# Kernel optimization log

Hardware: AMD Instinct MI355X
Metric: run time of the kernel (lower is better)

Reference implementation:

```python
import jax, jax.numpy as jnp
import numpy as np
import math

B, C, H, W = 16, 512, 32, 32
HEADS = 8
HD = C // HEADS            # 64 head_dim
NFREQ = HD // 4            # 16 (head_dim % 4 == 0)
MAX_FREQ = 128.0
T = H * W                  # 1024 tokens


def _make_so2_mat():
    # make_2dcoord: meshgrid('ij') of arange(H), arange(W) -> [H, W, 2]
    xg, yg = np.meshgrid(np.arange(H, dtype=np.float32), np.arange(W, dtype=np.float32), indexing='ij')
    coord = np.stack([xg, yg], -1)                                   # [H, W, 2]
    freqs = np.exp(np.linspace(0.0, math.log(MAX_FREQ), NFREQ)).astype(np.float32)  # [NFREQ]
    th = coord[..., None, :] * freqs[None, None, :, None]            # [H, W, NFREQ, 2]
    c, s = np.cos(th), np.sin(th)
    # rotation matrices [[c, -s], [s, c]] -> [H, W, NFREQ, 2(dim), 2, 2]
    mat = np.stack([np.stack([c, -s], -1), np.stack([s, c], -1)], -2)
    mat = mat.reshape(H * W, NFREQ * 2, 2, 2)                        # flatten(2,3) then flatten(0,1)
    return jnp.asarray(mat[:, : HD // 2])                            # [T, HD//2, 2, 2]


def setup_inputs() -> dict:
    key = jax.random.key(0)
    ks = jax.random.split(key, 5)
    mat = _make_so2_mat()
    return {
        'x': jax.random.normal(ks[0], (B, C, H, W), dtype=jnp.float32),
        'w_qkv': jax.random.normal(ks[1], (3 * C, C), dtype=jnp.float32) * 0.02,
        'b_qkv': jax.random.normal(ks[2], (3 * C,), dtype=jnp.float32) * 0.02,
        'w_o': jax.random.normal(ks[3], (C, C), dtype=jnp.float32) * 0.02,
        'b_o': jax.random.normal(ks[4], (C,), dtype=jnp.float32) * 0.02,
        'mat_q': mat,
        'mat_k': mat,
        'mat_v': mat,
        'mat_o': jnp.swapaxes(mat, -2, -1),
    }


def _rep_mul(rep, t):
    # rep: [T, HD//2, 2, 2]; t: [B, nh, T, HD] -> per-pair 2x2 rotation
    tb = t.reshape(B, HEADS, T, HD // 2, 2)
    return jnp.einsum('tfij,bntfj->bntfi', rep, tb).reshape(B, HEADS, T, HD)


def _split_heads(t):
    # 'b (c nh) h w -> b nh (h w) c' (c outer, nh inner in channel dim)
    return t.reshape(B, HD, HEADS, T).transpose(0, 2, 3, 1)


def reference(x, w_qkv, b_qkv, w_o, b_o, mat_q, mat_k, mat_v, mat_o):
    # 1x1 conv QKV projection == channel GEMM
    qkv = jnp.einsum('bchw,oc->bohw', x, w_qkv) + b_qkv[None, :, None, None]
    q, k, v = jnp.split(qkv, 3, axis=1)
    q, k, v = map(_split_heads, (q, k, v))                 # [B, nh, T, HD]
    q = _rep_mul(mat_q, q)
    k = _rep_mul(mat_k, k)
    v = _rep_mul(mat_v, v)
    scale = 1.0 / math.sqrt(HD)
    attn = jax.nn.softmax(jnp.einsum('bntd,bnsd->bnts', q, k) * scale, axis=-1)
    o = jnp.einsum('bnts,bnsd->bntd', attn, v)             # [B, nh, T, HD]
    o = _rep_mul(mat_o, o)
    # 'b nh (h w) c -> b (c nh) h w'
    o = o.reshape(B, HEADS, H, W, HD).transpose(0, 4, 1, 2, 3).reshape(B, C, H, W)
    return jnp.einsum('bchw,oc->bohw', o, w_o) + b_o[None, :, None, None]
```

## Files before the change

kernel.cpp:

```cpp
#include <hip/hip_runtime.h>


typedef __bf16 bf16x8 __attribute__((ext_vector_type(8)));
typedef __bf16 bf16x4 __attribute__((ext_vector_type(4)));
typedef float  f32x4  __attribute__((ext_vector_type(4)));

__device__ __forceinline__ f32x4 mfma16(bf16x8 a, bf16x8 b, f32x4 c) {
    return __builtin_amdgcn_mfma_f32_16x16x32_bf16(a, b, c, 0, 0, 0);
}

__device__ __forceinline__ void async16(const void* g, void* l) {
    __builtin_amdgcn_global_load_lds(
        (const __attribute__((address_space(1))) void*)g,
        (__attribute__((address_space(3))) void*)l, 16, 0, 0);
}

__global__ void k_convert_w(const float* __restrict__ wq, const float* __restrict__ wo,
                            __bf16* __restrict__ wqb, __bf16* __restrict__ wob) {
    int i = blockIdx.x * 256 + threadIdx.x;
    if (i < 3 * 512 * 512) wqb[i] = (__bf16)wq[i];
    if (i < 512 * 512) {
        int o = i >> 9, k2 = i & 511;
        int nh = k2 >> 6, hd = k2 & 63;
        wob[i] = (__bf16)wo[o * 512 + hd * 8 + nh];
    }
}

__global__ void k_transpose_x(const float* __restrict__ x, __bf16* __restrict__ xt) {
    __shared__ float tile[64][65];
    const int b  = blockIdx.z;
    const int c0 = blockIdx.y * 64;
    const int t0 = blockIdx.x * 64;
    const int tx = threadIdx.x, ty = threadIdx.y;
    const float* xp = x + ((size_t)b * 512 + c0) * 1024 + t0;
#pragma unroll
    for (int j = 0; j < 16; j++)
        tile[ty + j * 4][tx] = xp[(ty + j * 4) * 1024 + tx];
    __syncthreads();
    __bf16* xo = xt + ((size_t)b * 1024 + t0) * 512 + c0;
#pragma unroll
    for (int j = 0; j < 16; j++)
        xo[(ty + j * 4) * 512 + tx] = (__bf16)tile[tx][ty + j * 4];
}

__global__ __launch_bounds__(512) void k_gemm_qkv(
        const __bf16* __restrict__ A, const __bf16* __restrict__ W,
        const float* __restrict__ bias,
        const float* __restrict__ matq, const float* __restrict__ matk,
        const float* __restrict__ matv,
        __bf16* __restrict__ qd, __bf16* __restrict__ kd, __bf16* __restrict__ vtd)
{
    __shared__ __bf16 As[2][128][64];
    __shared__ __bf16 Bs[2][256][64];
    const int tid = threadIdx.x;
    const int m0 = blockIdx.x * 128;
    const int jb = blockIdx.y;
    const int part = jb >> 1;
    const int nh_base = (jb & 1) * 4;
    const int lane = tid & 63, w = tid >> 6;
    const int ln = lane & 15, quad = lane >> 4;
    const int wr = w >> 2, wc = w & 3;

    const int srow = lane >> 3;
    const int scol = (((lane & 7) ^ srow) * 8);

    const __bf16* arow[2];
    const __bf16* brow[4];
#pragma unroll
    for (int jj = 0; jj < 2; jj++) {
        int rr = w * 16 + jj * 8 + srow;
        arow[jj] = &A[(size_t)(m0 + rr) * 512 + scol];
    }
#pragma unroll
    for (int jj = 0; jj < 4; jj++) {
        int rr = w * 32 + jj * 8 + srow;
        int o = part * 512 + (rr & 63) * 8 + nh_base + (rr >> 6);
        brow[jj] = &W[(size_t)o * 512 + scol];
    }

    f32x4 acc[4][4] = {};

#define STAGE_QKV(T, BUF)                                                   \
    do {                                                                    \
        const int _k0 = (T) * 64;                                           \
        _Pragma("unroll")                                                   \
        for (int jj = 0; jj < 2; jj++)                                      \
            async16(arow[jj] + _k0, &As[BUF][w * 16 + jj * 8][0]);          \
        _Pragma("unroll")                                                   \
        for (int jj = 0; jj < 4; jj++)                                      \
            async16(brow[jj] + _k0, &Bs[BUF][w * 32 + jj * 8][0]);          \
    } while (0)

    STAGE_QKV(0, 0);
    STAGE_QKV(1, 1);
    asm volatile("s_waitcnt vmcnt(6)" ::: "memory");
    __builtin_amdgcn_s_barrier();

#pragma unroll
    for (int t = 0; t < 8; ++t) {
        const int cur = t & 1;
        bf16x8 af[2][4], wf[2][4];
#pragma unroll
        for (int h = 0; h < 2; h++) {
#pragma unroll
            for (int mi = 0; mi < 4; mi++)
                af[h][mi] = *(const bf16x8*)&As[cur][wr * 64 + mi * 16 + ln][(((h * 4 + quad) ^ (ln & 7)) * 8)];
#pragma unroll
            for (int ni = 0; ni < 4; ni++)
                wf[h][ni] = *(const bf16x8*)&Bs[cur][wc * 64 + ni * 16 + ln][(((h * 4 + quad) ^ (ln & 7)) * 8)];
        }
        asm volatile("s_waitcnt lgkmcnt(0)" ::: "memory");
        __builtin_amdgcn_sched_barrier(0);
        __builtin_amdgcn_s_barrier();
        if (t < 6) STAGE_QKV(t + 2, cur);
        __builtin_amdgcn_s_setprio(1);
#pragma unroll
        for (int h = 0; h < 2; h++)
#pragma unroll
            for (int mi = 0; mi < 4; mi++)
#pragma unroll
                for (int ni = 0; ni < 4; ni++)
                    acc[mi][ni] = mfma16(af[h][mi], wf[h][ni], acc[mi][ni]);
        __builtin_amdgcn_s_setprio(0);
        if (t < 6) { asm volatile("s_waitcnt vmcnt(6)" ::: "memory"); }
        else       { asm volatile("s_waitcnt vmcnt(0)" ::: "memory"); }
        __builtin_amdgcn_s_barrier();
    }
#undef STAGE_QKV

    const int nh = nh_base + wc;
    const int rowbase = m0 + wr * 64;
    const int b  = rowbase >> 10, t0 = rowbase & 1023;
    const int bh = b * 8 + nh;
    const int ip = ln & 1;
    const float2* matp = (const float2*)(part == 0 ? matq : (part == 1 ? matk : matv));
    __bf16* qkdst = (part == 0) ? qd : kd;
    const float qscale = (part == 0) ? 0.18033688011112042f : 1.0f;

#pragma unroll
    for (int ni = 0; ni < 4; ni++) {
        const int hd = ni * 16 + ln;
        const int f  = hd >> 1;
        const float bias_o = bias[part * 512 + hd * 8 + nh];
#pragma unroll
        for (int mi = 0; mi < 4; mi++) {
            const int tq = t0 + mi * 16 + quad * 4;
            if (part < 2) {
#pragma unroll
                for (int r = 0; r < 4; r++) {
                    int t = tq + r;
                    float val = acc[mi][ni][r] + bias_o;
                    float pr  = __shfl_xor(val, 1);
                    float2 mv = matp[((size_t)t * 32 + f) * 2 + ip];
                    float e  = ip ? pr : val;
                    float oo = ip ? val : pr;
                    float rv = (mv.x * e + mv.y * oo) * qscale;
                    qkdst[((size_t)bh * 1024 + t) * 64 + hd] = (__bf16)rv;
                }
            } else {
                __bf16 pack[4];
#pragma unroll
                for (int r = 0; r < 4; r++) {
                    int t = tq + r;
                    float val = acc[mi][ni][r] + bias_o;
                    float pr  = __shfl_xor(val, 1);
                    float2 mv = matp[((size_t)t * 32 + f) * 2 + ip];
                    float e  = ip ? pr : val;
                    float oo = ip ? val : pr;
                    pack[r] = (__bf16)(mv.x * e + mv.y * oo);
                }
                *(uint2*)&vtd[((size_t)bh * 64 + hd) * 1024 + tq] = *(const uint2*)pack;
            }
        }
    }
}

__global__ __launch_bounds__(512) void k_attn(
        const __bf16* __restrict__ q, const __bf16* __restrict__ kk,
        const __bf16* __restrict__ vt, const float* __restrict__ mato,
        __bf16* __restrict__ od)
{
    __shared__ __bf16 Ks[64][64];
    __shared__ __bf16 Vs[64][64];
    __shared__ __bf16 Ps[8][32][64];
    const int bh = blockIdx.x, qt = blockIdx.y;
    const int tid = threadIdx.x, w = tid >> 6, lane = tid & 63;
    const int ln = lane & 15, quad = lane >> 4;
    const int lx = ln & 7;
    const int srow = lane >> 3;
    const int scol = ((lane & 7) ^ srow) * 8;
    const int qr0 = qt * 256 + w * 32;

    bf16x8 qa[2][2];
#pragma unroll
    for (int mi = 0; mi < 2; mi++)
#pragma unroll
        for (int ki = 0; ki < 2; ki++)
            qa[mi][ki] = *(const bf16x8*)&q[((size_t)bh * 1024 + qr0 + mi * 16 + ln) * 64 + ki * 32 + quad * 8];

    const __bf16* kbase = kk + (size_t)bh * 1024 * 64;
    const __bf16* vbase = vt + (size_t)bh * 64 * 1024;

    f32x4 oacc[2][4] = {};
    f32x4 lacc[2] = {};

    bf16x8 ones;
#pragma unroll
    for (int j = 0; j < 8; j++) ones[j] = (__bf16)1.0f;

    for (int st = 0; st < 16; st++) {
        async16(kbase + (size_t)(st * 64 + w * 8 + srow) * 64 + scol, &Ks[w * 8][0]);
        async16(vbase + (size_t)(w * 8 + srow) * 1024 + st * 64 + scol, &Vs[w * 8][0]);
        __syncthreads();

#pragma unroll
        for (int si = 0; si < 4; si++) {
            bf16x8 kb0 = *(const bf16x8*)&Ks[si * 16 + ln][((quad    ) ^ lx) * 8];
            bf16x8 kb1 = *(const bf16x8*)&Ks[si * 16 + ln][((quad + 4) ^ lx) * 8];
            f32x4 sc[2] = {};
#pragma unroll
            for (int mi = 0; mi < 2; mi++) {
                sc[mi] = mfma16(kb0, qa[mi][0], sc[mi]);
                sc[mi] = mfma16(kb1, qa[mi][1], sc[mi]);
            }
#pragma unroll
            for (int mi = 0; mi < 2; mi++) {
                bf16x4 pk;
#pragma unroll
                for (int r = 0; r < 4; r++)
                    pk[r] = (__bf16)exp2f(sc[mi][r]);
                *(bf16x4*)((char*)&Ps[w][mi * 16 + ln][0]
                           + (((si * 2 + (quad >> 1)) ^ lx) * 16) + (quad & 1) * 8) = pk;
            }
        }

#pragma unroll
        for (int kt = 0; kt < 2; kt++) {
            bf16x8 pa[2];
#pragma unroll
            for (int mi = 0; mi < 2; mi++)
                pa[mi] = *(const bf16x8*)&Ps[w][mi * 16 + ln][((kt * 4 + quad) ^ lx) * 8];
#pragma unroll
            for (int ni = 0; ni < 4; ni++) {
                bf16x8 vb = *(const bf16x8*)&Vs[ni * 16 + ln][((kt * 4 + quad) ^ lx) * 8];
                oacc[0][ni] = mfma16(vb, pa[0], oacc[0][ni]);
                oacc[1][ni] = mfma16(vb, pa[1], oacc[1][ni]);
            }
            lacc[0] = mfma16(ones, pa[0], lacc[0]);
            lacc[1] = mfma16(ones, pa[1], lacc[1]);
        }
        __syncthreads();
    }

    const float4* mo4 = (const float4*)mato;
#pragma unroll
    for (int mi = 0; mi < 2; mi++) {
        const int t = qr0 + mi * 16 + ln;
        const float invl = 1.0f / lacc[mi][0];
#pragma unroll
        for (int ni = 0; ni < 4; ni++) {
            const int hd0 = ni * 16 + quad * 4;
            const int f   = hd0 >> 1;
            float v0 = oacc[mi][ni][0] * invl;
            float v1 = oacc[mi][ni][1] * invl;
            float v2 = oacc[mi][ni][2] * invl;
            float v3 = oacc[mi][ni][3] * invl;
            float4 m1 = mo4[(size_t)t * 32 + f];
            float4 m2 = mo4[(size_t)t * 32 + f + 1];
            __bf16 pk[4];
            pk[0] = (__bf16)(m1.x * v0 + m1.y * v1);
            pk[1] = (__bf16)(m1.z * v0 + m1.w * v1);
            pk[2] = (__bf16)(m2.x * v2 + m2.y * v3);
            pk[3] = (__bf16)(m2.z * v2 + m2.w * v3);
            *(uint2*)&od[((size_t)bh * 1024 + t) * 64 + hd0] = *(const uint2*)pk;
        }
    }
}

__global__ __launch_bounds__(512) void k_gemm_out(
        const __bf16* __restrict__ A, const __bf16* __restrict__ W,
        const float* __restrict__ bias, float* __restrict__ out)
{
    __shared__ __bf16 As[2][128][64];
    __shared__ __bf16 Bs[2][256][64];
    const int tid = threadIdx.x;
    const int m0 = blockIdx.x * 128;
    const int n0 = blockIdx.y * 256;
    const int lane = tid & 63, w = tid >> 6;
    const int ln = lane & 15, quad = lane >> 4;
    const int wr = w >> 2, wc = w & 3;

    const int srow = lane >> 3;
    const int scol = (((lane & 7) ^ srow) * 8);

    const int bb = m0 >> 10, t00 = m0 & 1023;

    const __bf16* arow[2];
    const __bf16* brow[4];
#pragma unroll
    for (int jj = 0; jj < 2; jj++) {
        int rr = w * 16 + jj * 8 + srow;
        arow[jj] = &A[((size_t)bb * 8192 + t00 + rr) * 64 + scol];
    }
#pragma unroll
    for (int jj = 0; jj < 4; jj++) {
        int rr = w * 32 + jj * 8 + srow;
        brow[jj] = &W[(size_t)(n0 + rr) * 512 + scol];
    }

    f32x4 acc[4][4] = {};

#define STAGE_OUT(T, BUF)                                                   \
    do {                                                                    \
        const int _k0 = (T) * 64;                                           \
        _Pragma("unroll")                                                   \
        for (int jj = 0; jj < 2; jj++)                                      \
            async16(arow[jj] + (size_t)_k0 * 1024, &As[BUF][w * 16 + jj * 8][0]); \
        _Pragma("unroll")                                                   \
        for (int jj = 0; jj < 4; jj++)                                      \
            async16(brow[jj] + _k0, &Bs[BUF][w * 32 + jj * 8][0]);          \
    } while (0)

    STAGE_OUT(0, 0);
    STAGE_OUT(1, 1);
    asm volatile("s_waitcnt vmcnt(6)" ::: "memory");
    __builtin_amdgcn_s_barrier();

#pragma unroll
    for (int t = 0; t < 8; ++t) {
        const int cur = t & 1;
        bf16x8 af[2][4], wf[2][4];
#pragma unroll
        for (int h = 0; h < 2; h++) {
#pragma unroll
            for (int mi = 0; mi < 4; mi++)
                af[h][mi] = *(const bf16x8*)&As[cur][wr * 64 + mi * 16 + ln][(((h * 4 + quad) ^ (ln & 7)) * 8)];
#pragma unroll
            for (int ni = 0; ni < 4; ni++)
                wf[h][ni] = *(const bf16x8*)&Bs[cur][wc * 64 + ni * 16 + ln][(((h * 4 + quad) ^ (ln & 7)) * 8)];
        }
        asm volatile("s_waitcnt lgkmcnt(0)" ::: "memory");
        __builtin_amdgcn_sched_barrier(0);
        __builtin_amdgcn_s_barrier();
        if (t < 6) STAGE_OUT(t + 2, cur);
        __builtin_amdgcn_s_setprio(1);
#pragma unroll
        for (int h = 0; h < 2; h++)
#pragma unroll
            for (int mi = 0; mi < 4; mi++)
#pragma unroll
                for (int ni = 0; ni < 4; ni++)
                    acc[mi][ni] = mfma16(af[h][mi], wf[h][ni], acc[mi][ni]);
        __builtin_amdgcn_s_setprio(0);
        if (t < 6) { asm volatile("s_waitcnt vmcnt(6)" ::: "memory"); }
        else       { asm volatile("s_waitcnt vmcnt(0)" ::: "memory"); }
        __builtin_amdgcn_s_barrier();
    }
#undef STAGE_OUT

    const int rowbase = m0 + wr * 64;
    const int bb2 = rowbase >> 10, t0 = rowbase & 1023;
#pragma unroll
    for (int ni = 0; ni < 4; ni++) {
        int o = n0 + wc * 64 + ni * 16 + ln;
        float bias_o = bias[o];
#pragma unroll
        for (int mi = 0; mi < 4; mi++) {
            int t = t0 + mi * 16 + quad * 4;
            f32x4 v = acc[mi][ni];
            v[0] += bias_o; v[1] += bias_o; v[2] += bias_o; v[3] += bias_o;
            *(f32x4*)&out[((size_t)bb2 * 512 + o) * 1024 + t] = v;
        }
    }
}

extern "C" void kernel_launch(void* const* d_in, const int* in_sizes, int n_in,
                              void* d_out, int out_size, void* d_ws, size_t ws_size,
                              hipStream_t stream) {
    (void)in_sizes; (void)n_in; (void)out_size; (void)ws_size;
    const float* x     = (const float*)d_in[0];
    const float* w_qkv = (const float*)d_in[1];
    const float* b_qkv = (const float*)d_in[2];
    const float* w_o   = (const float*)d_in[3];
    const float* b_o   = (const float*)d_in[4];
    const float* mat_q = (const float*)d_in[5];
    const float* mat_k = (const float*)d_in[6];
    const float* mat_v = (const float*)d_in[7];
    const float* mat_o = (const float*)d_in[8];
    float* out = (float*)d_out;

    char* p = (char*)d_ws;
    __bf16* wqb = (__bf16*)p;  p += (size_t)3 * 512 * 512 * 2;
    __bf16* wob = (__bf16*)p;  p += (size_t)512 * 512 * 2;
    char* xt_base = p;
    __bf16* xt  = (__bf16*)p;  p += (size_t)16384 * 512 * 2;
    __bf16* qd  = (__bf16*)p;  p += (size_t)128 * 1024 * 64 * 2;
    __bf16* kd  = (__bf16*)p;  p += (size_t)128 * 1024 * 64 * 2;
    __bf16* vtd = (__bf16*)p;  p += (size_t)128 * 64 * 1024 * 2;
    __bf16* od  = (__bf16*)xt_base;

    k_convert_w  <<<dim3(3072),       dim3(256),    0, stream>>>(w_qkv, w_o, wqb, wob);
    k_transpose_x<<<dim3(16, 8, 16),  dim3(64, 4),  0, stream>>>(x, xt);
    k_gemm_qkv   <<<dim3(128, 6),     dim3(512),    0, stream>>>(xt, wqb, b_qkv, mat_q, mat_k, mat_v, qd, kd, vtd);
    k_attn       <<<dim3(128, 4),     dim3(512),    0, stream>>>(qd, kd, vtd, mat_o, od);
    k_gemm_out   <<<dim3(128, 2),     dim3(512),    0, stream>>>(od, wob, b_o, out);
}
```

Measured before the change: 223.8 us.

## Triple-buffer attention K/V loads, halve query tile, and remap blocks for XCD locality

New measurement: 233.4 us. 4.3% more time.

```diff
diff --git a/kernel.cpp b/kernel.cpp
--- a/kernel.cpp
+++ b/kernel.cpp
@@ -53,8 +53,10 @@
     __shared__ __bf16 As[2][128][64];
     __shared__ __bf16 Bs[2][256][64];
     const int tid = threadIdx.x;
-    const int m0 = blockIdx.x * 128;
-    const int jb = blockIdx.y;
+    const int id = blockIdx.x;
+    const int logical = (id >> 3) + (id & 7) * 96;
+    const int m0 = (logical / 6) * 128;
+    const int jb = logical % 6;
     const int part = jb >> 1;
     const int nh_base = (jb & 1) * 4;
     const int lane = tid & 63, w = tid >> 6;
@@ -180,100 +182,103 @@
         const __bf16* __restrict__ vt, const float* __restrict__ mato,
         __bf16* __restrict__ od)
 {
-    __shared__ __bf16 Ks[64][64];
-    __shared__ __bf16 Vs[64][64];
-    __shared__ __bf16 Ps[8][32][64];
-    const int bh = blockIdx.x, qt = blockIdx.y;
+    __shared__ __bf16 Ks[3][64][64];
+    __shared__ __bf16 Vs[3][64][64];
+    __shared__ __bf16 Ps[8][16][64];
+    const int id = blockIdx.x;
+    const int logical = (id >> 3) + (id & 7) * 128;
+    const int bh = logical >> 3, qt = logical & 7;
     const int tid = threadIdx.x, w = tid >> 6, lane = tid & 63;
     const int ln = lane & 15, quad = lane >> 4;
     const int lx = ln & 7;
     const int srow = lane >> 3;
     const int scol = ((lane & 7) ^ srow) * 8;
-    const int qr0 = qt * 256 + w * 32;
-
-    bf16x8 qa[2][2];
-#pragma unroll
-    for (int mi = 0; mi < 2; mi++)
-#pragma unroll
-        for (int ki = 0; ki < 2; ki++)
-            qa[mi][ki] = *(const bf16x8*)&q[((size_t)bh * 1024 + qr0 + mi * 16 + ln) * 64 + ki * 32 + quad * 8];
+    const int qr0 = qt * 128 + w * 16;
+
+    bf16x8 qa[2];
+#pragma unroll
+    for (int ki = 0; ki < 2; ki++)
+        qa[ki] = *(const bf16x8*)&q[((size_t)bh * 1024 + qr0 + ln) * 64 + ki * 32 + quad * 8];
 
     const __bf16* kbase = kk + (size_t)bh * 1024 * 64;
     const __bf16* vbase = vt + (size_t)bh * 64 * 1024;
 
-    f32x4 oacc[2][4] = {};
-    f32x4 lacc[2] = {};
+    f32x4 oacc[4] = {};
+    f32x4 lacc = {};
 
     bf16x8 ones;
 #pragma unroll
     for (int j = 0; j < 8; j++) ones[j] = (__bf16)1.0f;
 
+#define STAGE_KV(T, BUF)                                                        \
+    do {                                                                        \
+        async16(kbase + (size_t)((T) * 64 + w * 8 + srow) * 64 + scol,          \
+                &Ks[BUF][w * 8][0]);                                            \
+        async16(vbase + (size_t)(w * 8 + srow) * 1024 + (T) * 64 + scol,        \
+                &Vs[BUF][w * 8][0]);                                            \
+    } while (0)
+
+    STAGE_KV(0, 0);
+    STAGE_KV(1, 1);
+
     for (int st = 0; st < 16; st++) {
-        async16(kbase + (size_t)(st * 64 + w * 8 + srow) * 64 + scol, &Ks[w * 8][0]);
-        async16(vbase + (size_t)(w * 8 + srow) * 1024 + st * 64 + scol, &Vs[w * 8][0]);
-        __syncthreads();
+        const int bf = st % 3;
+        if (st < 14) STAGE_KV(st + 2, (st + 2) % 3);
+        if (st <= 13)      { asm volatile("s_waitcnt vmcnt(4)" ::: "memory"); }
+        else if (st == 14) { asm volatile("s_waitcnt vmcnt(2)" ::: "memory"); }
+        else               { asm volatile("s_waitcnt vmcnt(0)" ::: "memory"); }
+        __builtin_amdgcn_s_barrier();
 
 #pragma unroll
         for (int si = 0; si < 4; si++) {
-            bf16x8 kb0 = *(const bf16x8*)&Ks[si * 16 + ln][((quad    ) ^ lx) * 8];
-            bf16x8 kb1 = *(const bf16x8*)&Ks[si * 16 + ln][((quad + 4) ^ lx) * 8];
-            f32x4 sc[2] = {};
-#pragma unroll
-            for (int mi = 0; mi < 2; mi++) {
-                sc[mi] = mfma16(kb0, qa[mi][0], sc[mi]);
-                sc[mi] = mfma16(kb1, qa[mi][1], sc[mi]);
+            bf16x8 kb0 = *(const bf16x8*)&Ks[bf][si * 16 + ln][((quad    ) ^ lx) * 8];
+            bf16x8 kb1 = *(const bf16x8*)&Ks[bf][si * 16 + ln][((quad + 4) ^ lx) * 8];
+            f32x4 sc = {};
+            sc = mfma16(kb0, qa[0], sc);
+            sc = mfma16(kb1, qa[1], sc);
+            bf16x4 pk;
+#pragma unroll
+            for (int r = 0; r < 4; r++)
+                pk[r] = (__bf16)exp2f(sc[r]);
+            *(bf16x4*)((char*)&Ps[w][ln][0]
+                       + (((si * 2 + (quad >> 1)) ^ lx) * 16) + (quad & 1) * 8) = pk;
+        }
+
+#pragma unroll
+        for (int kt = 0; kt < 2; kt++) {
+            bf16x8 pa = *(const bf16x8*)&Ps[w][ln][((kt * 4 + quad) ^ lx) * 8];
+#pragma unroll
+            for (int ni = 0; ni < 4; ni++) {
+                bf16x8 vb = *(const bf16x8*)&Vs[bf][ni * 16 + ln][((kt * 4 + quad) ^ lx) * 8];
+                oacc[ni] = mfma16(vb, pa, oacc[ni]);
             }
-#pragma unroll
-            for (int mi = 0; mi < 2; mi++) {
-                bf16x4 pk;
-#pragma unroll
-                for (int r = 0; r < 4; r++)
-                    pk[r] = (__bf16)exp2f(sc[mi][r]);
-                *(bf16x4*)((char*)&Ps[w][mi * 16 + ln][0]
-                           + (((si * 2 + (quad >> 1)) ^ lx) * 16) + (quad & 1) * 8) = pk;
-            }
-        }
-
-#pragma unroll
-        for (int kt = 0; kt < 2; kt++) {
-            bf16x8 pa[2];
-#pragma unroll
-            for (int mi = 0; mi < 2; mi++)
-                pa[mi] = *(const bf16x8*)&Ps[w][mi * 16 + ln][((kt * 4 + quad) ^ lx) * 8];
-#pragma unroll
-            for (int ni = 0; ni < 4; ni++) {
-                bf16x8 vb = *(const bf16x8*)&Vs[ni * 16 + ln][((kt * 4 + quad) ^ lx) * 8];
-                oacc[0][ni] = mfma16(vb, pa[0], oacc[0][ni]);
-                oacc[1][ni] = mfma16(vb, pa[1], oacc[1][ni]);
-            }
-            lacc[0] = mfma16(ones, pa[0], lacc[0]);
-            lacc[1] = mfma16(ones, pa[1], lacc[1]);
-        }
-        __syncthreads();
-    }
-
+            lacc = mfma16(ones, pa, lacc);
+        }
+        asm volatile("s_waitcnt lgkmcnt(0)" ::: "memory");
+        __builtin_amdgcn_sched_barrier(0);
+        __builtin_amdgcn_s_barrier();
+    }
+#undef STAGE_KV
+
+    const float invl = 1.0f / lacc[0];
     const float4* mo4 = (const float4*)mato;
-#pragma unroll
-    for (int mi = 0; mi < 2; mi++) {
-        const int t = qr0 + mi * 16 + ln;
-        const float invl = 1.0f / lacc[mi][0];
-#pragma unroll
-        for (int ni = 0; ni < 4; ni++) {
-            const int hd0 = ni * 16 + quad * 4;
-            const int f   = hd0 >> 1;
-            float v0 = oacc[mi][ni][0] * invl;
-            float v1 = oacc[mi][ni][1] * invl;
-            float v2 = oacc[mi][ni][2] * invl;
-            float v3 = oacc[mi][ni][3] * invl;
-            float4 m1 = mo4[(size_t)t * 32 + f];
-            float4 m2 = mo4[(size_t)t * 32 + f + 1];
-            __bf16 pk[4];
-            pk[0] = (__bf16)(m1.x * v0 + m1.y * v1);
-            pk[1] = (__bf16)(m1.z * v0 + m1.w * v1);
-            pk[2] = (__bf16)(m2.x * v2 + m2.y * v3);
-            pk[3] = (__bf16)(m2.z * v2 + m2.w * v3);
-            *(uint2*)&od[((size_t)bh * 1024 + t) * 64 + hd0] = *(const uint2*)pk;
-        }
+    const int t = qr0 + ln;
+#pragma unroll
+    for (int ni = 0; ni < 4; ni++) {
+        const int hd0 = ni * 16 + quad * 4;
+        const int f   = hd0 >> 1;
+        float v0 = oacc[ni][0] * invl;
+        float v1 = oacc[ni][1] * invl;
+        float v2 = oacc[ni][2] * invl;
+        float v3 = oacc[ni][3] * invl;
+        float4 m1 = mo4[(size_t)t * 32 + f];
+        float4 m2 = mo4[(size_t)t * 32 + f + 1];
+        __bf16 pk[4];
+        pk[0] = (__bf16)(m1.x * v0 + m1.y * v1);
+        pk[1] = (__bf16)(m1.z * v0 + m1.w * v1);
+        pk[2] = (__bf16)(m2.x * v2 + m2.y * v3);
+        pk[3] = (__bf16)(m2.z * v2 + m2.w * v3);
+        *(uint2*)&od[((size_t)bh * 1024 + t) * 64 + hd0] = *(const uint2*)pk;
     }
 }
 
@@ -284,8 +289,10 @@
     __shared__ __bf16 As[2][128][64];
     __shared__ __bf16 Bs[2][256][64];
     const int tid = threadIdx.x;
-    const int m0 = blockIdx.x * 128;
-    const int n0 = blockIdx.y * 256;
+    const int id = blockIdx.x;
+    const int logical = (id >> 3) + (id & 7) * 32;
+    const int m0 = (logical >> 1) * 128;
+    const int n0 = (logical & 1) * 256;
     const int lane = tid & 63, w = tid >> 6;
     const int ln = lane & 15, quad = lane >> 4;
     const int wr = w >> 2, wc = w & 3;
@@ -401,7 +408,7 @@
 
     k_convert_w  <<<dim3(3072),       dim3(256),    0, stream>>>(w_qkv, w_o, wqb, wob);
     k_transpose_x<<<dim3(16, 8, 16),  dim3(64, 4),  0, stream>>>(x, xt);
-    k_gemm_qkv   <<<dim3(128, 6),     dim3(512),    0, stream>>>(xt, wqb, b_qkv, mat_q, mat_k, mat_v, qd, kd, vtd);
-    k_attn       <<<dim3(128, 4),     dim3(512),    0, stream>>>(qd, kd, vtd, mat_o, od);
-    k_gemm_out   <<<dim3(128, 2),     dim3(512),    0, stream>>>(od, wob, b_o, out);
-}
+    k_gemm_qkv   <<<dim3(768),        dim3(512),    0, stream>>>(xt, wqb, b_qkv, mat_q, mat_k, mat_v, qd, kd, vtd);
+    k_attn       <<<dim3(1024),       dim3(512),    0, stream>>>(qd, kd, vtd, mat_o, od);
+    k_gemm_out   <<<dim3(256),        dim3(512),    0, stream>>>(od, wob, b_o, out);
+}
```
